# Optimization experiments

Measured on AMD Instinct MI355X. Metric: run time of the kernel, lower is better.

The kernel has to match this reference:

```python
import jax, jax.numpy as jnp
import numpy as np
import math

S, B, D = 2048, 8, 256
HEADS = 8
DPROJ = 128
DFF = 1024
DH = DPROJ // HEADS  # 16


def _layernorm(x, g, b, eps=1e-5):
    mu = jnp.mean(x, axis=-1, keepdims=True)
    var = jnp.mean((x - mu) ** 2, axis=-1, keepdims=True)
    return (x - mu) * jax.lax.rsqrt(var + eps) * g + b


def setup_inputs() -> dict:
    key = jax.random.key(0)
    ks = jax.random.split(key, 16)
    s = 0.02
    return {
        "src": jax.random.normal(ks[0], (S, B, D), dtype=jnp.float32),
        "Wq": jax.random.normal(ks[1], (D, DPROJ), dtype=jnp.float32) * s,
        "bq": jnp.zeros((DPROJ,), dtype=jnp.float32),
        "Wk": jax.random.normal(ks[2], (D, DPROJ), dtype=jnp.float32) * s,
        "bk": jnp.zeros((DPROJ,), dtype=jnp.float32),
        "Wv": jax.random.normal(ks[3], (D, DPROJ), dtype=jnp.float32) * s,
        "bv": jnp.zeros((DPROJ,), dtype=jnp.float32),
        "Wo": jax.random.normal(ks[4], (DPROJ, D), dtype=jnp.float32) * s,
        "ln1_g": jnp.ones((D,), dtype=jnp.float32),
        "ln1_b": jnp.zeros((D,), dtype=jnp.float32),
        "W1": jax.random.normal(ks[5], (D, DFF), dtype=jnp.float32) * s,
        "b1": jnp.zeros((DFF,), dtype=jnp.float32),
        "W2": jax.random.normal(ks[6], (DFF, D), dtype=jnp.float32) * s,
        "b2": jnp.zeros((D,), dtype=jnp.float32),
        "ln2_g": jnp.ones((D,), dtype=jnp.float32),
        "ln2_b": jnp.zeros((D,), dtype=jnp.float32),
    }


def reference(src, Wq, bq, Wk, bk, Wv, bv, Wo, ln1_g, ln1_b, W1, b1, W2, b2, ln2_g, ln2_b):
    # src: (S, B, D)
    q = src @ Wq + bq  # (S, B, DPROJ)
    k = src @ Wk + bk
    v = src @ Wv + bv

    # _reshape_to_batches: (S, B, h*dh) -> (S, B*h, dh), then sdpa moves batch first
    def split_heads(x):
        return jnp.transpose(x.reshape(S, B * HEADS, DH), (1, 0, 2))  # (B*h, S, dh)

    qh, kh, vh = split_heads(q), split_heads(k), split_heads(v)
    scores = jnp.einsum('bid,bjd->bij', qh, kh) / math.sqrt(DH)  # (B*h, S, S)
    attn = jax.nn.softmax(scores, axis=-1)
    ctx = jnp.einsum('bij,bjd->bid', attn, vh)  # (B*h, S, dh)

    # _reshape_from_batches: (B*h, S, dh) -> (S, B, DPROJ)
    ctx = jnp.transpose(ctx, (1, 0, 2)).reshape(S, B, DPROJ)
    y = ctx @ Wo  # (S, B, D), no bias

    x = _layernorm(src + y, ln1_g, ln1_b)
    ffn = jax.nn.relu(x @ W1 + b1) @ W2 + b2
    return _layernorm(x + ffn, ln2_g, ln2_b)
```

## Files before the change

kernel.cpp:

```cpp
#include <hip/hip_runtime.h>
#include <math.h>

#define SLEN 2048
#define BATCH 8
#define DMODEL 256
#define HEADS 8
#define DPROJ 128
#define DFF 1024
#define DH 16
#define MROWS (SLEN*BATCH)

typedef unsigned short u16;
typedef unsigned int u32;
typedef __attribute__((ext_vector_type(8))) short short8;
typedef __attribute__((ext_vector_type(4))) float f32x4;
typedef __attribute__((ext_vector_type(4))) unsigned short u16x4;

__device__ __forceinline__ u16 f2bf(float x) {
    union { float f; u32 u; } v; v.f = x;
    u32 r = v.u + 0x7FFFu + ((v.u >> 16) & 1u);
    return (u16)(r >> 16);
}
__device__ __forceinline__ float fexp2(float x) { return __builtin_amdgcn_exp2f(x); }
__device__ __forceinline__ u32 pack_bf(float lo, float hi) {
    union { float f; u32 u; } a, b; a.f = lo; b.f = hi;
    return __builtin_amdgcn_perm(b.u, a.u, 0x07060302u);
}

__global__ void conv_src_kernel(const float* __restrict__ src, u16* __restrict__ dst) {
    int idx = (blockIdx.x * 256 + threadIdx.x) * 4;
    float4 v = *(const float4*)(src + idx);
    u16x4 o;
    o.x = f2bf(v.x); o.y = f2bf(v.y); o.z = f2bf(v.z); o.w = f2bf(v.w);
    *(u16x4*)(dst + idx) = o;
}

__global__ void conv_wts_kernel(const float* __restrict__ Wq, const float* __restrict__ Wk,
                                const float* __restrict__ Wv, const float* __restrict__ Wo,
                                const float* __restrict__ W1, const float* __restrict__ W2,
                                u16* __restrict__ WqT, u16* __restrict__ WkT,
                                u16* __restrict__ WvT, u16* __restrict__ WoT,
                                u16* __restrict__ W1T, u16* __restrict__ W2T) {
    int i = blockIdx.x * 256 + threadIdx.x;
    if (i < 32768) {
        int n = i >> 8, k = i & 255;
        WqT[i] = f2bf(Wq[k * 128 + n]);
    } else if (i < 65536) {
        int j = i - 32768; int n = j >> 8, k = j & 255;
        WkT[j] = f2bf(Wk[k * 128 + n]);
    } else if (i < 98304) {
        int j = i - 65536; int n = j >> 8, k = j & 255;
        WvT[j] = f2bf(Wv[k * 128 + n]);
    } else if (i < 131072) {
        int j = i - 98304; int n = j >> 7, k = j & 127;
        WoT[j] = f2bf(Wo[k * 256 + n]);
    } else if (i < 393216) {
        int j = i - 131072; int n = j >> 8, k = j & 255;
        W1T[j] = f2bf(W1[k * 1024 + n]);
    } else if (i < 655360) {
        int j = i - 393216; int n = j >> 10, k = j & 1023;
        W2T[j] = f2bf(W2[k * 256 + n]);
    }
}

template<int BN, bool RELU, bool HAS_BIAS, bool OUT_BF16>
__global__ void mfma_gemm(const u16* __restrict__ A, const u16* __restrict__ BT,
                          const float* __restrict__ bias, void* __restrict__ Cout,
                          int M, int N, int K) {
    constexpr int NJ = BN / 32;
    __shared__ __align__(16) u16 As[128 * 40];
    __shared__ __align__(16) u16 Bs[BN * 40];
    const int tid = threadIdx.x;
    const int row0 = blockIdx.x * 128;
    const int col0 = blockIdx.y * BN;
    const int w = tid >> 6, l = tid & 63;
    const int wr = (w & 1) * 64, wc = (w >> 1) * (BN / 2);
    const int lcol = l & 15, lrow = (l >> 4) * 4, kq = (l >> 4) * 8;
    const int sr = tid >> 2;
    const int sc = (tid & 3) * 8;

    f32x4 acc[4][NJ] = {};
    for (int k0 = 0; k0 < K; k0 += 32) {
        *(uint4*)(As + sr * 40 + sc) =
            *(const uint4*)(A + (size_t)(row0 + sr) * K + k0 + sc);
        *(uint4*)(As + (sr + 64) * 40 + sc) =
            *(const uint4*)(A + (size_t)(row0 + sr + 64) * K + k0 + sc);
        *(uint4*)(Bs + sr * 40 + sc) =
            *(const uint4*)(BT + (size_t)(col0 + sr) * K + k0 + sc);
        if (BN == 128)
            *(uint4*)(Bs + (sr + 64) * 40 + sc) =
                *(const uint4*)(BT + (size_t)(col0 + sr + 64) * K + k0 + sc);
        __syncthreads();
        short8 af[4], bf[NJ];
        #pragma unroll
        for (int i = 0; i < 4; ++i)
            af[i] = *(const short8*)(As + (wr + i * 16 + lcol) * 40 + kq);
        #pragma unroll
        for (int j = 0; j < NJ; ++j)
            bf[j] = *(const short8*)(Bs + (wc + j * 16 + lcol) * 40 + kq);
        #pragma unroll
        for (int i = 0; i < 4; ++i)
            #pragma unroll
            for (int j = 0; j < NJ; ++j)
                acc[i][j] = __builtin_amdgcn_mfma_f32_16x16x32_bf16(
                    af[i], bf[j], acc[i][j], 0, 0, 0);
        __syncthreads();
    }
    float bv[NJ];
    #pragma unroll
    for (int j = 0; j < NJ; ++j)
        bv[j] = HAS_BIAS ? bias[col0 + wc + j * 16 + lcol] : 0.f;
    #pragma unroll
    for (int i = 0; i < 4; ++i) {
        #pragma unroll
        for (int r = 0; r < 4; ++r) {
            size_t grow = row0 + wr + i * 16 + lrow + r;
            #pragma unroll
            for (int j = 0; j < NJ; ++j) {
                int gcol = col0 + wc + j * 16 + lcol;
                float c = acc[i][j][r] + bv[j];
                if (RELU) c = fmaxf(c, 0.f);
                if (OUT_BF16) ((u16*)Cout)[grow * N + gcol] = f2bf(c);
                else          ((float*)Cout)[grow * N + gcol] = c;
            }
        }
    }
}

__global__ void qkv_mfma(const u16* __restrict__ A,
                         const u16* __restrict__ WqT, const u16* __restrict__ WkT,
                         const u16* __restrict__ WvT,
                         const float* __restrict__ bq, const float* __restrict__ bk,
                         const float* __restrict__ bv,
                         u16* __restrict__ qhp, u16* __restrict__ khp,
                         u16* __restrict__ vhb) {
    const int which = blockIdx.z;
    const u16* BT   = which == 0 ? WqT : (which == 1 ? WkT : WvT);
    const float* bs = which == 0 ? bq : (which == 1 ? bk : bv);
    const float scale = which == 0 ? 0.25f * 1.44269504f : 1.0f;
    __shared__ __align__(16) u16 As[128 * 40];
    __shared__ __align__(16) u16 Bs[128 * 40];
    const int tid = threadIdx.x;
    const int row0 = blockIdx.x * 128;
    const int w = tid >> 6, l = tid & 63;
    const int wr = (w & 1) * 64, wc = (w >> 1) * 64;
    const int lcol = l & 15, lrow = (l >> 4) * 4, kq = (l >> 4) * 8;
    const int sr = tid >> 2;
    const int sc = (tid & 3) * 8;

    f32x4 acc[4][4] = {};
    for (int k0 = 0; k0 < DMODEL; k0 += 32) {
        *(uint4*)(As + sr * 40 + sc) =
            *(const uint4*)(A + (size_t)(row0 + sr) * DMODEL + k0 + sc);
        *(uint4*)(As + (sr + 64) * 40 + sc) =
            *(const uint4*)(A + (size_t)(row0 + sr + 64) * DMODEL + k0 + sc);
        *(uint4*)(Bs + sr * 40 + sc) =
            *(const uint4*)(BT + (size_t)sr * DMODEL + k0 + sc);
        *(uint4*)(Bs + (sr + 64) * 40 + sc) =
            *(const uint4*)(BT + (size_t)(sr + 64) * DMODEL + k0 + sc);
        __syncthreads();
        short8 af[4], bf[4];
        #pragma unroll
        for (int i = 0; i < 4; ++i)
            af[i] = *(const short8*)(As + (wr + i * 16 + lcol) * 40 + kq);
        #pragma unroll
        for (int j = 0; j < 4; ++j)
            bf[j] = *(const short8*)(Bs + (wc + j * 16 + lcol) * 40 + kq);
        #pragma unroll
        for (int i = 0; i < 4; ++i)
            #pragma unroll
            for (int j = 0; j < 4; ++j)
                acc[i][j] = __builtin_amdgcn_mfma_f32_16x16x32_bf16(
                    af[i], bf[j], acc[i][j], 0, 0, 0);
        __syncthreads();
    }
    #pragma unroll
    for (int i = 0; i < 4; ++i) {
        #pragma unroll
        for (int r = 0; r < 4; ++r) {
            int grow = row0 + wr + i * 16 + lrow + r;
            int b = grow & 7, s = grow >> 3;
            #pragma unroll
            for (int j = 0; j < 4; ++j) {
                int gcol = wc + j * 16 + lcol;
                int h = gcol >> 4, d = gcol & 15;
                float c = acc[i][j][r] + bs[gcol];
                if (which == 2) {
                    vhb[((size_t)(b * 8 + h) * SLEN + s) * 16 + d] = f2bf(c);
                } else {
                    u16* base = (which == 0 ? qhp : khp)
                              + ((size_t)(b * 8 + h) * SLEN + s) * 32;
                    base[d] = f2bf(c * scale);
                    base[d + 16] = 0;
                }
            }
        }
    }
}

__global__ void transpose_v(const u16* __restrict__ vhb, u16* __restrict__ vT) {
    __shared__ u16 T[128 * 24];
    const int bh = blockIdx.y;
    const int c0 = blockIdx.x * 128;
    const int t = threadIdx.x;
    {
        int key = t >> 1, half = t & 1;
        *(uint4*)(T + key * 24 + half * 8) =
            *(const uint4*)(vhb + ((size_t)bh * SLEN + c0 + key) * 16 + half * 8);
    }
    __syncthreads();
    int d = t >> 4, k8 = (t & 15) * 8;
    u16x4 o0, o1;
    o0.x = T[(k8 + 0) * 24 + d]; o0.y = T[(k8 + 1) * 24 + d];
    o0.z = T[(k8 + 2) * 24 + d]; o0.w = T[(k8 + 3) * 24 + d];
    o1.x = T[(k8 + 4) * 24 + d]; o1.y = T[(k8 + 5) * 24 + d];
    o1.z = T[(k8 + 6) * 24 + d]; o1.w = T[(k8 + 7) * 24 + d];
    u16* dst = vT + ((size_t)bh * 16 + d) * SLEN + c0 + k8;
    *(u16x4*)dst = o0;
    *(u16x4*)(dst + 4) = o1;
}

__global__ __launch_bounds__(256, 4)
void attn_mfma(const u16* __restrict__ qg, const u16* __restrict__ kg,
               const u16* __restrict__ vT, u16* __restrict__ ctx) {
    __shared__ __align__(16) u16 Ps[4 * 32 * 70];
    const int bh = blockIdx.y;
    const int q0 = blockIdx.x * 128;
    const int tid = threadIdx.x;
    const int w = tid >> 6, l = tid & 63;
    const int qc = l & 15, g = l >> 4;
    u16* Pw = Ps + w * (32 * 70);

    short8 qf[2];
    {
        const u16* qbase = qg + ((size_t)bh * SLEN + q0 + w * 32) * 32;
        qf[0] = *(const short8*)(qbase + qc * 32 + 8 * g);
        qf[1] = *(const short8*)(qbase + (16 + qc) * 32 + 8 * g);
    }
    const u16* kbase = kg + (size_t)bh * SLEN * 32;
    const u16* vbase = vT + ((size_t)bh * 16 + qc) * SLEN;

    f32x4 o_[2] = {};
    f32x4 ls[2] = {};
    const short one_bf = (short)0x3F80;
    short8 onesB = {one_bf, one_bf, one_bf, one_bf, one_bf, one_bf, one_bf, one_bf};

    for (int k0 = 0; k0 < SLEN; k0 += 64) {
        short8 kf[4], vf[2];
        #pragma unroll
        for (int kj = 0; kj < 4; ++kj)
            kf[kj] = *(const short8*)(kbase + (size_t)(k0 + kj * 16 + qc) * 32 + 8 * g);
        #pragma unroll
        for (int ks = 0; ks < 2; ++ks)
            vf[ks] = *(const short8*)(vbase + k0 + ks * 32 + 8 * g);

        f32x4 s_[4][2];
        #pragma unroll
        for (int kj = 0; kj < 4; ++kj)
            #pragma unroll
            for (int mi = 0; mi < 2; ++mi) {
                f32x4 z = {0.f, 0.f, 0.f, 0.f};
                s_[kj][mi] = __builtin_amdgcn_mfma_f32_16x16x32_bf16(
                    kf[kj], qf[mi], z, 0, 0, 0);
            }
        #pragma unroll
        for (int mi = 0; mi < 2; ++mi)
            #pragma unroll
            for (int kj = 0; kj < 4; ++kj) {
                f32x4 sv = s_[kj][mi];
                u32 d0 = pack_bf(fexp2(sv[0]), fexp2(sv[1]));
                u32 d1 = pack_bf(fexp2(sv[2]), fexp2(sv[3]));
                u32* pp = (u32*)(Pw + (mi * 16 + qc) * 70 + kj * 16 + 4 * g);
                pp[0] = d0;
                pp[1] = d1;
            }
        #pragma unroll
        for (int ks = 0; ks < 2; ++ks) {
            #pragma unroll
            for (int mi = 0; mi < 2; ++mi) {
                const u32* rp = (const u32*)(Pw + (mi * 16 + qc) * 70 + ks * 32 + 8 * g);
                union { u32 d[4]; short8 v; } ap;
                ap.d[0] = rp[0]; ap.d[1] = rp[1]; ap.d[2] = rp[2]; ap.d[3] = rp[3];
                o_[mi] = __builtin_amdgcn_mfma_f32_16x16x32_bf16(ap.v, vf[ks], o_[mi], 0, 0, 0);
                ls[mi] = __builtin_amdgcn_mfma_f32_16x16x32_bf16(ap.v, onesB, ls[mi], 0, 0, 0);
            }
        }
    }
    const int b = bh >> 3, h = bh & 7;
    #pragma unroll
    for (int mi = 0; mi < 2; ++mi)
        #pragma unroll
        for (int r = 0; r < 4; ++r) {
            int qrow = q0 + w * 32 + mi * 16 + 4 * g + r;
            ctx[((size_t)qrow * BATCH + b) * DPROJ + h * DH + qc] =
                f2bf(o_[mi][r] / ls[mi][r]);
        }
}

__device__ __forceinline__ float bf2f(u16 h) {
    union { u32 u; float f; } v; v.u = ((u32)h) << 16;
    return v.f;
}
__global__ void ln1_kernel(const float* __restrict__ src, const u16* __restrict__ y,
                           const float* __restrict__ g, const float* __restrict__ bb,
                           u16* __restrict__ xb) {
    const int w = threadIdx.x >> 6, l = threadIdx.x & 63;
    const int row = blockIdx.x * 4 + w;
    const int c = l * 4;
    size_t base = (size_t)row * DMODEL;
    float4 s4 = *(const float4*)(src + base + c);
    u16x4 y4 = *(const u16x4*)(y + base + c);
    float v[4] = { s4.x + bf2f(y4.x), s4.y + bf2f(y4.y),
                   s4.z + bf2f(y4.z), s4.w + bf2f(y4.w) };
    float sum = v[0] + v[1] + v[2] + v[3];
    float ss  = v[0]*v[0] + v[1]*v[1] + v[2]*v[2] + v[3]*v[3];
    #pragma unroll
    for (int off = 1; off < 64; off <<= 1) {
        sum += __shfl_xor(sum, off);
        ss  += __shfl_xor(ss, off);
    }
    float mu = sum * (1.0f / 256.0f);
    float var = ss * (1.0f / 256.0f) - mu * mu;
    float rs = rsqrtf(var + 1e-5f);
    float4 g4 = *(const float4*)(g + c);
    float4 b4 = *(const float4*)(bb + c);
    u16x4 o;
    o.x = f2bf((v[0] - mu) * rs * g4.x + b4.x);
    o.y = f2bf((v[1] - mu) * rs * g4.y + b4.y);
    o.z = f2bf((v[2] - mu) * rs * g4.z + b4.z);
    o.w = f2bf((v[3] - mu) * rs * g4.w + b4.w);
    *(u16x4*)(xb + base + c) = o;
}

__global__ void ln2_kernel(const u16* __restrict__ x, const u16* __restrict__ f,
                           const float* __restrict__ g, const float* __restrict__ bb,
                           float* __restrict__ out) {
    const int w = threadIdx.x >> 6, l = threadIdx.x & 63;
    const int row = blockIdx.x * 4 + w;
    const int c = l * 4;
    size_t base = (size_t)row * DMODEL;
    u16x4 x4 = *(const u16x4*)(x + base + c);
    u16x4 f4 = *(const u16x4*)(f + base + c);
    float v[4] = { bf2f(x4.x) + bf2f(f4.x), bf2f(x4.y) + bf2f(f4.y),
                   bf2f(x4.z) + bf2f(f4.z), bf2f(x4.w) + bf2f(f4.w) };
    float sum = v[0] + v[1] + v[2] + v[3];
    float ss  = v[0]*v[0] + v[1]*v[1] + v[2]*v[2] + v[3]*v[3];
    #pragma unroll
    for (int off = 1; off < 64; off <<= 1) {
        sum += __shfl_xor(sum, off);
        ss  += __shfl_xor(ss, off);
    }
    float mu = sum * (1.0f / 256.0f);
    float var = ss * (1.0f / 256.0f) - mu * mu;
    float rs = rsqrtf(var + 1e-5f);
    float4 g4 = *(const float4*)(g + c);
    float4 b4 = *(const float4*)(bb + c);
    float4 o;
    o.x = (v[0] - mu) * rs * g4.x + b4.x;
    o.y = (v[1] - mu) * rs * g4.y + b4.y;
    o.z = (v[2] - mu) * rs * g4.z + b4.z;
    o.w = (v[3] - mu) * rs * g4.w + b4.w;
    *(float4*)(out + base + c) = o;
}

extern "C" void kernel_launch(void* const* d_in, const int* in_sizes, int n_in,
                              void* d_out, int out_size, void* d_ws, size_t ws_size,
                              hipStream_t stream) {
    const float* src = (const float*)d_in[0];
    const float* Wq  = (const float*)d_in[1];
    const float* bq  = (const float*)d_in[2];
    const float* Wk  = (const float*)d_in[3];
    const float* bk  = (const float*)d_in[4];
    const float* Wv  = (const float*)d_in[5];
    const float* bv  = (const float*)d_in[6];
    const float* Wo  = (const float*)d_in[7];
    const float* g1  = (const float*)d_in[8];
    const float* be1 = (const float*)d_in[9];
    const float* W1  = (const float*)d_in[10];
    const float* b1  = (const float*)d_in[11];
    const float* W2  = (const float*)d_in[12];
    const float* b2  = (const float*)d_in[13];
    const float* g2  = (const float*)d_in[14];
    const float* be2 = (const float*)d_in[15];
    char* ws = (char*)d_ws;
    float* out = (float*)d_out;

    u16* qhp  = (u16*)(ws + 0);
    u16* khp  = (u16*)(ws + 8388608);
    u16* vhb  = (u16*)(ws + 16777216);
    u16* vT   = (u16*)(ws + 20971520);
    u16* ctxb = (u16*)(ws + 25165824);
    u16* yb   = (u16*)(ws + 29360128);
    u16* hb   = (u16*)(ws + 0);
    u16* xb   = (u16*)(ws + 37748736);
    u16* fb   = (u16*)(ws + 46137344);
    u16* srcb = (u16*)(ws + 54525952);
    u16* WqT  = (u16*)(ws + 62914560);
    u16* WkT  = (u16*)(ws + 62980096);
    u16* WvT  = (u16*)(ws + 63045632);
    u16* WoT  = (u16*)(ws + 63111168);
    u16* W1T  = (u16*)(ws + 63176704);
    u16* W2T  = (u16*)(ws + 63700992);

    conv_src_kernel<<<4096, 256, 0, stream>>>(src, srcb);
    conv_wts_kernel<<<2560, 256, 0, stream>>>(Wq, Wk, Wv, Wo, W1, W2,
                                              WqT, WkT, WvT, WoT, W1T, W2T);
    qkv_mfma<<<dim3(128, 1, 3), 256, 0, stream>>>(srcb, WqT, WkT, WvT,
                                                  bq, bk, bv, qhp, khp, vhb);
    transpose_v<<<dim3(16, 64), 256, 0, stream>>>(vhb, vT);
    attn_mfma<<<dim3(16, 64), 256, 0, stream>>>(qhp, khp, vT, ctxb);
    mfma_gemm<64, false, false, true><<<dim3(128, 4), 256, 0, stream>>>(
        ctxb, WoT, nullptr, yb, MROWS, DMODEL, DPROJ);
    ln1_kernel<<<MROWS / 4, 256, 0, stream>>>(src, yb, g1, be1, xb);
    mfma_gemm<128, true, true, true><<<dim3(128, 8), 256, 0, stream>>>(
        xb, W1T, b1, hb, MROWS, DFF, DMODEL);
    mfma_gemm<64, false, true, true><<<dim3(128, 4), 256, 0, stream>>>(
        hb, W2T, b2, fb, MROWS, DMODEL, DFF);
    ln2_kernel<<<MROWS / 4, 256, 0, stream>>>(xb, fb, g2, be2, out);
}
```

Measured before the change: 235.9 us.

## Use direct global-to-LDS loads with XOR swizzle, double-buffer attention P, merge prep kernels

The GEMM and QKV kernels now stage tiles into LDS with global_load_lds 16-byte loads, replacing the register round-trip. Because these loads cannot pad rows, padded LDS rows are swapped for an XOR-swizzled layout to avoid bank conflicts. The attention kernel double-buffers its per-wave P tile, pads rows to 76 and uses 8-byte LDS accesses. The two conversion kernels are merged into one launch. The changes cut load latency, bank conflicts and launch overhead, at the cost of more LDS in attention and reliance on the swizzle layout being correct.

```diff
diff --git a/kernel.cpp b/kernel.cpp
--- a/kernel.cpp
+++ b/kernel.cpp
@@ -21,27 +21,37 @@
     u32 r = v.u + 0x7FFFu + ((v.u >> 16) & 1u);
     return (u16)(r >> 16);
 }
+__device__ __forceinline__ float bf2f(u16 h) {
+    union { u32 u; float f; } v; v.u = ((u32)h) << 16;
+    return v.f;
+}
 __device__ __forceinline__ float fexp2(float x) { return __builtin_amdgcn_exp2f(x); }
 __device__ __forceinline__ u32 pack_bf(float lo, float hi) {
     union { float f; u32 u; } a, b; a.f = lo; b.f = hi;
     return __builtin_amdgcn_perm(b.u, a.u, 0x07060302u);
 }
-
-__global__ void conv_src_kernel(const float* __restrict__ src, u16* __restrict__ dst) {
-    int idx = (blockIdx.x * 256 + threadIdx.x) * 4;
-    float4 v = *(const float4*)(src + idx);
-    u16x4 o;
-    o.x = f2bf(v.x); o.y = f2bf(v.y); o.z = f2bf(v.z); o.w = f2bf(v.w);
-    *(u16x4*)(dst + idx) = o;
-}
-
-__global__ void conv_wts_kernel(const float* __restrict__ Wq, const float* __restrict__ Wk,
-                                const float* __restrict__ Wv, const float* __restrict__ Wo,
-                                const float* __restrict__ W1, const float* __restrict__ W2,
-                                u16* __restrict__ WqT, u16* __restrict__ WkT,
-                                u16* __restrict__ WvT, u16* __restrict__ WoT,
-                                u16* __restrict__ W1T, u16* __restrict__ W2T) {
-    int i = blockIdx.x * 256 + threadIdx.x;
+__device__ __forceinline__ void gld16(const u16* g, u16* l) {
+    __builtin_amdgcn_global_load_lds(
+        (const __attribute__((address_space(1))) void*)g,
+        (__attribute__((address_space(3))) void*)l, 16, 0, 0);
+}
+
+__global__ void prep_kernel(const float* __restrict__ src, u16* __restrict__ srcb,
+                            const float* __restrict__ Wq, const float* __restrict__ Wk,
+                            const float* __restrict__ Wv, const float* __restrict__ Wo,
+                            const float* __restrict__ W1, const float* __restrict__ W2,
+                            u16* __restrict__ WqT, u16* __restrict__ WkT,
+                            u16* __restrict__ WvT, u16* __restrict__ WoT,
+                            u16* __restrict__ W1T, u16* __restrict__ W2T) {
+    if (blockIdx.x < 4096) {
+        int idx = (blockIdx.x * 256 + threadIdx.x) * 4;
+        float4 v = *(const float4*)(src + idx);
+        u16x4 o;
+        o.x = f2bf(v.x); o.y = f2bf(v.y); o.z = f2bf(v.z); o.w = f2bf(v.w);
+        *(u16x4*)(srcb + idx) = o;
+        return;
+    }
+    int i = (blockIdx.x - 4096) * 256 + threadIdx.x;
     if (i < 32768) {
         int n = i >> 8, k = i & 255;
         WqT[i] = f2bf(Wq[k * 128 + n]);
@@ -68,36 +78,41 @@
                           const float* __restrict__ bias, void* __restrict__ Cout,
                           int M, int N, int K) {
     constexpr int NJ = BN / 32;
-    __shared__ __align__(16) u16 As[128 * 40];
-    __shared__ __align__(16) u16 Bs[BN * 40];
+    __shared__ __align__(16) u16 As[128 * 32];
+    __shared__ __align__(16) u16 Bs[BN * 32];
     const int tid = threadIdx.x;
     const int row0 = blockIdx.x * 128;
     const int col0 = blockIdx.y * BN;
     const int w = tid >> 6, l = tid & 63;
     const int wr = (w & 1) * 64, wc = (w >> 1) * (BN / 2);
-    const int lcol = l & 15, lrow = (l >> 4) * 4, kq = (l >> 4) * 8;
-    const int sr = tid >> 2;
-    const int sc = (tid & 3) * 8;
+    const int lcol = l & 15, lrow = (l >> 4) * 4, g = l >> 4;
+    const int sl = l >> 2;
+    const int swc = ((l & 3) ^ (sl & 3)) * 8;
+    const int fsw = (g ^ (lcol & 3)) * 8;
+
+    const u16* Ag0 = A + (size_t)(row0 + 16 * w + sl) * K + swc;
+    const u16* Ag1 = Ag0 + (size_t)64 * K;
+    const u16* Bg0 = BT + (size_t)(col0 + 16 * w + sl) * K + swc;
+    const u16* Bg1 = Bg0 + (size_t)64 * K;
+    u16* lA0 = As + (16 * w) * 32;
+    u16* lA1 = As + (16 * w + 64) * 32;
+    u16* lB0 = Bs + (16 * w) * 32;
+    u16* lB1 = Bs + (16 * w + 64) * 32;
 
     f32x4 acc[4][NJ] = {};
     for (int k0 = 0; k0 < K; k0 += 32) {
-        *(uint4*)(As + sr * 40 + sc) =
-            *(const uint4*)(A + (size_t)(row0 + sr) * K + k0 + sc);
-        *(uint4*)(As + (sr + 64) * 40 + sc) =
-            *(const uint4*)(A + (size_t)(row0 + sr + 64) * K + k0 + sc);
-        *(uint4*)(Bs + sr * 40 + sc) =
-            *(const uint4*)(BT + (size_t)(col0 + sr) * K + k0 + sc);
-        if (BN == 128)
-            *(uint4*)(Bs + (sr + 64) * 40 + sc) =
-                *(const uint4*)(BT + (size_t)(col0 + sr + 64) * K + k0 + sc);
+        gld16(Ag0 + k0, lA0);
+        gld16(Ag1 + k0, lA1);
+        gld16(Bg0 + k0, lB0);
+        if (BN == 128) gld16(Bg1 + k0, lB1);
         __syncthreads();
         short8 af[4], bf[NJ];
         #pragma unroll
         for (int i = 0; i < 4; ++i)
-            af[i] = *(const short8*)(As + (wr + i * 16 + lcol) * 40 + kq);
+            af[i] = *(const short8*)(As + (wr + i * 16 + lcol) * 32 + fsw);
         #pragma unroll
         for (int j = 0; j < NJ; ++j)
-            bf[j] = *(const short8*)(Bs + (wc + j * 16 + lcol) * 40 + kq);
+            bf[j] = *(const short8*)(Bs + (wc + j * 16 + lcol) * 32 + fsw);
         #pragma unroll
         for (int i = 0; i < 4; ++i)
             #pragma unroll
@@ -138,34 +153,40 @@
     const u16* BT   = which == 0 ? WqT : (which == 1 ? WkT : WvT);
     const float* bs = which == 0 ? bq : (which == 1 ? bk : bv);
     const float scale = which == 0 ? 0.25f * 1.44269504f : 1.0f;
-    __shared__ __align__(16) u16 As[128 * 40];
-    __shared__ __align__(16) u16 Bs[128 * 40];
+    __shared__ __align__(16) u16 As[128 * 32];
+    __shared__ __align__(16) u16 Bs[128 * 32];
     const int tid = threadIdx.x;
     const int row0 = blockIdx.x * 128;
     const int w = tid >> 6, l = tid & 63;
     const int wr = (w & 1) * 64, wc = (w >> 1) * 64;
-    const int lcol = l & 15, lrow = (l >> 4) * 4, kq = (l >> 4) * 8;
-    const int sr = tid >> 2;
-    const int sc = (tid & 3) * 8;
+    const int lcol = l & 15, lrow = (l >> 4) * 4, g = l >> 4;
+    const int sl = l >> 2;
+    const int swc = ((l & 3) ^ (sl & 3)) * 8;
+    const int fsw = (g ^ (lcol & 3)) * 8;
+
+    const u16* Ag0 = A + (size_t)(row0 + 16 * w + sl) * DMODEL + swc;
+    const u16* Ag1 = Ag0 + (size_t)64 * DMODEL;
+    const u16* Bg0 = BT + (size_t)(16 * w + sl) * DMODEL + swc;
+    const u16* Bg1 = Bg0 + (size_t)64 * DMODEL;
+    u16* lA0 = As + (16 * w) * 32;
+    u16* lA1 = As + (16 * w + 64) * 32;
+    u16* lB0 = Bs + (16 * w) * 32;
+    u16* lB1 = Bs + (16 * w + 64) * 32;
 
     f32x4 acc[4][4] = {};
     for (int k0 = 0; k0 < DMODEL; k0 += 32) {
-        *(uint4*)(As + sr * 40 + sc) =
-            *(const uint4*)(A + (size_t)(row0 + sr) * DMODEL + k0 + sc);
-        *(uint4*)(As + (sr + 64) * 40 + sc) =
-            *(const uint4*)(A + (size_t)(row0 + sr + 64) * DMODEL + k0 + sc);
-        *(uint4*)(Bs + sr * 40 + sc) =
-            *(const uint4*)(BT + (size_t)sr * DMODEL + k0 + sc);
-        *(uint4*)(Bs + (sr + 64) * 40 + sc) =
-            *(const uint4*)(BT + (size_t)(sr + 64) * DMODEL + k0 + sc);
+        gld16(Ag0 + k0, lA0);
+        gld16(Ag1 + k0, lA1);
+        gld16(Bg0 + k0, lB0);
+        gld16(Bg1 + k0, lB1);
         __syncthreads();
         short8 af[4], bf[4];
         #pragma unroll
         for (int i = 0; i < 4; ++i)
-            af[i] = *(const short8*)(As + (wr + i * 16 + lcol) * 40 + kq);
+            af[i] = *(const short8*)(As + (wr + i * 16 + lcol) * 32 + fsw);
         #pragma unroll
         for (int j = 0; j < 4; ++j)
-            bf[j] = *(const short8*)(Bs + (wc + j * 16 + lcol) * 40 + kq);
+            bf[j] = *(const short8*)(Bs + (wc + j * 16 + lcol) * 32 + fsw);
         #pragma unroll
         for (int i = 0; i < 4; ++i)
             #pragma unroll
@@ -223,13 +244,14 @@
 __global__ __launch_bounds__(256, 4)
 void attn_mfma(const u16* __restrict__ qg, const u16* __restrict__ kg,
                const u16* __restrict__ vT, u16* __restrict__ ctx) {
-    __shared__ __align__(16) u16 Ps[4 * 32 * 70];
+    __shared__ __align__(16) u16 Ps[2 * 4 * 32 * 76];
     const int bh = blockIdx.y;
     const int q0 = blockIdx.x * 128;
     const int tid = threadIdx.x;
     const int w = tid >> 6, l = tid & 63;
     const int qc = l & 15, g = l >> 4;
-    u16* Pw = Ps + w * (32 * 70);
+    u16* Pw0 = Ps + w * 2432;
+    u16* Pw1 = Ps + 9728 + w * 2432;
 
     short8 qf[2];
     {
@@ -245,7 +267,10 @@
     const short one_bf = (short)0x3F80;
     short8 onesB = {one_bf, one_bf, one_bf, one_bf, one_bf, one_bf, one_bf, one_bf};
 
-    for (int k0 = 0; k0 < SLEN; k0 += 64) {
+    #pragma unroll 2
+    for (int kt = 0; kt < 32; ++kt) {
+        const int k0 = kt * 64;
+        u16* Pw = (kt & 1) ? Pw1 : Pw0;
         short8 kf[4], vf[2];
         #pragma unroll
         for (int kj = 0; kj < 4; ++kj)
@@ -268,19 +293,19 @@
             #pragma unroll
             for (int kj = 0; kj < 4; ++kj) {
                 f32x4 sv = s_[kj][mi];
-                u32 d0 = pack_bf(fexp2(sv[0]), fexp2(sv[1]));
-                u32 d1 = pack_bf(fexp2(sv[2]), fexp2(sv[3]));
-                u32* pp = (u32*)(Pw + (mi * 16 + qc) * 70 + kj * 16 + 4 * g);
-                pp[0] = d0;
-                pp[1] = d1;
+                uint2 dd;
+                dd.x = pack_bf(fexp2(sv[0]), fexp2(sv[1]));
+                dd.y = pack_bf(fexp2(sv[2]), fexp2(sv[3]));
+                *(uint2*)(Pw + (mi * 16 + qc) * 76 + kj * 16 + 4 * g) = dd;
             }
         #pragma unroll
         for (int ks = 0; ks < 2; ++ks) {
             #pragma unroll
             for (int mi = 0; mi < 2; ++mi) {
-                const u32* rp = (const u32*)(Pw + (mi * 16 + qc) * 70 + ks * 32 + 8 * g);
-                union { u32 d[4]; short8 v; } ap;
-                ap.d[0] = rp[0]; ap.d[1] = rp[1]; ap.d[2] = rp[2]; ap.d[3] = rp[3];
+                const u16* rp = Pw + (mi * 16 + qc) * 76 + ks * 32 + 8 * g;
+                union { uint2 q[2]; short8 v; } ap;
+                ap.q[0] = *(const uint2*)rp;
+                ap.q[1] = *(const uint2*)(rp + 4);
                 o_[mi] = __builtin_amdgcn_mfma_f32_16x16x32_bf16(ap.v, vf[ks], o_[mi], 0, 0, 0);
                 ls[mi] = __builtin_amdgcn_mfma_f32_16x16x32_bf16(ap.v, onesB, ls[mi], 0, 0, 0);
             }
@@ -297,10 +322,6 @@
         }
 }
 
-__device__ __forceinline__ float bf2f(u16 h) {
-    union { u32 u; float f; } v; v.u = ((u32)h) << 16;
-    return v.f;
-}
 __global__ void ln1_kernel(const float* __restrict__ src, const u16* __restrict__ y,
                            const float* __restrict__ g, const float* __restrict__ bb,
                            u16* __restrict__ xb) {
@@ -402,9 +423,8 @@
     u16* W1T  = (u16*)(ws + 63176704);
     u16* W2T  = (u16*)(ws + 63700992);
 
-    conv_src_kernel<<<4096, 256, 0, stream>>>(src, srcb);
-    conv_wts_kernel<<<2560, 256, 0, stream>>>(Wq, Wk, Wv, Wo, W1, W2,
-                                              WqT, WkT, WvT, WoT, W1T, W2T);
+    prep_kernel<<<6656, 256, 0, stream>>>(src, srcb, Wq, Wk, Wv, Wo, W1, W2,
+                                          WqT, WkT, WvT, WoT, W1T, W2T);
     qkv_mfma<<<dim3(128, 1, 3), 256, 0, stream>>>(srcb, WqT, WkT, WvT,
                                                   bq, bk, bv, qhp, khp, vhb);
     transpose_v<<<dim3(16, 64), 256, 0, stream>>>(vhb, vT);
```

After: 231.4 us. Within noise of the previous version (-1.9%).
